# Kernel tuning notes

Measured on AMD Instinct MI355X. Metric: run time of the kernel, lower is better.

## Reference

```python
import jax, jax.numpy as jnp
import numpy as np

MEMORY_SIZE = 32768
FEATURE_DIM = 128
BATCH = 4096


def setup_inputs() -> dict:
    key = jax.random.key(0)
    k1, k2, k3, k4 = jax.random.split(key, 4)
    memory = jax.random.normal(k1, (MEMORY_SIZE, FEATURE_DIM), dtype=jnp.float32)
    input_data = jax.random.normal(k2, (BATCH, FEATURE_DIM), dtype=jnp.float32)
    write_weights = jax.random.uniform(k3, (BATCH, MEMORY_SIZE), dtype=jnp.float32)
    query = jax.random.normal(k4, (BATCH, FEATURE_DIM), dtype=jnp.float32)
    return {"memory": memory, "input_data": input_data,
            "write_weights": write_weights, "query": query}


def reference(memory, input_data, write_weights, query):
    # ---- write(): row-normalize weights, scatter-accumulate into memory ----
    # The original python double-loop computes update[j] += w[i,j] * x[i],
    # i.e. update = w_norm.T @ x  -- a single GEMM.
    w_norm = write_weights / jnp.sum(write_weights, axis=1, keepdims=True)
    update = jnp.einsum('bm,bf->mf', w_norm, input_data)  # [M, F]
    memory_new = memory + update

    # ---- read(): softmax attention over memory slots ----
    scores = jnp.matmul(query, memory_new.T)              # [B, M]
    attention_weights = jax.nn.softmax(scores, axis=1)
    retrieved_memory = jnp.matmul(attention_weights, memory_new)  # [B, F]
    confidence_scores = jnp.max(attention_weights, axis=1)        # [B]
    return retrieved_memory, confidence_scores, memory_new
```

## Files before the change

kernel.cpp:

```cpp
#include <hip/hip_runtime.h>
#include <hip/hip_bf16.h>
#include <math.h>

#define MEMSZ 32768
#define FDIM  128
#define BATCH 4096

typedef float f32x4 __attribute__((ext_vector_type(4)));
typedef _Float16 f16x8 __attribute__((ext_vector_type(8)));
typedef short bf16x8 __attribute__((ext_vector_type(8)));
typedef unsigned short u16t;
typedef unsigned int u32t;

static __device__ __forceinline__ u16t f2h_bits(float f) {
    union { _Float16 h; u16t u; } c;
    c.h = (_Float16)f;
    return c.u;
}

#define GLDS16(gsrc, ldst) \
  __builtin_amdgcn_global_load_lds((const __attribute__((address_space(1))) void*)(gsrc), \
                                   (__attribute__((address_space(3))) void*)(ldst), 16, 0, 0)

__global__ __launch_bounds__(256) void k_rowsum(const float* __restrict__ W,
                                                float* __restrict__ inv_s) {
    const int row = blockIdx.x;
    const float4* Wr = reinterpret_cast<const float4*>(W + (size_t)row * MEMSZ);
    float acc = 0.f;
    #pragma unroll 4
    for (int i = threadIdx.x; i < MEMSZ / 4; i += 256) {
        float4 v = Wr[i];
        acc += (v.x + v.y) + (v.z + v.w);
    }
    #pragma unroll
    for (int off = 32; off > 0; off >>= 1)
        acc += __shfl_down(acc, off, 64);
    __shared__ float wsum[4];
    const int lane = threadIdx.x & 63, wid = threadIdx.x >> 6;
    if (lane == 0) wsum[wid] = acc;
    __syncthreads();
    if (threadIdx.x == 0)
        inv_s[row] = 1.0f / (wsum[0] + wsum[1] + wsum[2] + wsum[3]);
}

__global__ __launch_bounds__(256) void k_prep(const float* __restrict__ X,
                                              const float* __restrict__ inv_s,
                                              unsigned char* __restrict__ XT64) {
    __shared__ float xs[64][132];
    const int T = blockIdx.x;
    const int b0 = T * 64;
    const int tid = threadIdx.x;
    #pragma unroll
    for (int i = 0; i < 8; ++i) {
        const int idx = tid + i * 256;
        const int row = idx >> 5, c4 = idx & 31;
        const float s = inv_s[b0 + row];
        float4 v = *reinterpret_cast<const float4*>(&X[(size_t)(b0 + row) * FDIM + c4 * 4]);
        v.x *= s; v.y *= s; v.z *= s; v.w *= s;
        *reinterpret_cast<float4*>(&xs[row][c4 * 4]) = v;
    }
    __syncthreads();
    #pragma unroll
    for (int i = 0; i < 4; ++i) {
        const int L = tid + i * 256;
        const int fh = L >> 9, ff = (L >> 7) & 3, ks = (L >> 6) & 1, ln = L & 63;
        const int f = fh * 64 + ff * 16 + (ln & 15);
        const int bi = ks * 32 + (ln >> 4) * 8;
        u32t pk[4];
        #pragma unroll
        for (int h = 0; h < 4; ++h) {
            const float lo = xs[bi + 2 * h][f];
            const float hi = xs[bi + 2 * h + 1][f];
            asm("v_cvt_pk_bf16_f32 %0, %1, %2" : "=v"(pk[h]) : "v"(lo), "v"(hi));
        }
        *reinterpret_cast<uint4*>(XT64 + (size_t)T * 16384 + (size_t)L * 16) =
            make_uint4(pk[0], pk[1], pk[2], pk[3]);
    }
}

#define K2B 64
#define K2M 64
__global__ __launch_bounds__(256, 2) void k_update_mfma(
    const float* __restrict__ W, const unsigned char* __restrict__ XT64,
    const float* __restrict__ Mem, float* __restrict__ MemNew,
    u16t* __restrict__ MemH, u16t* __restrict__ MemHT)
{
    __shared__ __align__(16) unsigned char wt[2][16384];

    const int tid = threadIdx.x;
    const int lane = tid & 63, w = tid >> 6;
    const int q16 = lane & 15, g = lane >> 4;
    const int wm = w >> 1, wf = w & 1;
    const int mblk = blockIdx.x * K2M;

    f32x4 acc[2][4];
    #pragma unroll
    for (int mf = 0; mf < 2; ++mf)
        #pragma unroll
        for (int ff = 0; ff < 4; ++ff) acc[mf][ff] = (f32x4){0.f, 0.f, 0.f, 0.f};

    const unsigned char* xbase = XT64 + (size_t)(wf * 8192 + lane * 16);

    auto stageW = [&](int buf, int t) {
        const int b0 = t * K2B;
        #pragma unroll
        for (int c = 0; c < 4; ++c) {
            const int gi = c * 256 + tid;
            const int b = gi >> 4;
            const int src = ((gi & 15) * 16) ^ ((b & 8) << 1);
            GLDS16((const unsigned char*)W + (size_t)(b0 + b) * (MEMSZ * 4) + (size_t)mblk * 4 + src,
                   &wt[buf][gi * 16]);
        }
    };
    auto loadB = [&](bf16x8 (&br)[4][2], int t) {
        const unsigned char* xp = xbase + (size_t)t * 16384;
        #pragma unroll
        for (int ff = 0; ff < 4; ++ff)
            #pragma unroll
            for (int ks = 0; ks < 2; ++ks)
                br[ff][ks] = *reinterpret_cast<const bf16x8*>(xp + ff * 2048 + ks * 1024);
    };
    auto compute = [&](int buf, bf16x8 (&br)[4][2]) {
        bf16x8 afr[2][2];
        const unsigned char* tb = &wt[buf][0];
        #pragma unroll
        for (int mf = 0; mf < 2; ++mf) {
            const int mm4 = (wm * 32 + mf * 16 + q16) * 4;
            #pragma unroll
            for (int ks = 0; ks < 2; ++ks) {
                float av[8];
                #pragma unroll
                for (int e = 0; e < 8; ++e) {
                    const int b = ks * 32 + g * 8 + e;
                    av[e] = *reinterpret_cast<const float*>(
                        tb + b * 256 + (mm4 ^ ((b & 8) << 1)));
                }
                union { u32t u[4]; bf16x8 v; } cv;
                #pragma unroll
                for (int h = 0; h < 4; ++h)
                    asm("v_cvt_pk_bf16_f32 %0, %1, %2" : "=v"(cv.u[h]) : "v"(av[2 * h]), "v"(av[2 * h + 1]));
                afr[mf][ks] = cv.v;
            }
        }
        #pragma unroll
        for (int mf = 0; mf < 2; ++mf)
            #pragma unroll
            for (int ff = 0; ff < 4; ++ff)
                #pragma unroll
                for (int ks = 0; ks < 2; ++ks)
                    acc[mf][ff] = __builtin_amdgcn_mfma_f32_16x16x32_bf16(
                        afr[mf][ks], br[ff][ks], acc[mf][ff], 0, 0, 0);
    };

    bf16x8 bA[4][2], bB_[4][2];
    stageW(0, 0); loadB(bA, 0);
    const int NT = BATCH / K2B;
    for (int t = 0; t < NT; t += 2) {
        __builtin_amdgcn_s_barrier();
        if (t + 1 < NT) { loadB(bB_, t + 1); stageW(1, t + 1); }
        if (t + 1 < NT) asm volatile("s_waitcnt vmcnt(12)" ::: "memory");
        else            asm volatile("s_waitcnt vmcnt(0)"  ::: "memory");
        __builtin_amdgcn_s_barrier();
        __builtin_amdgcn_sched_barrier(0);
        compute(0, bA);
        __builtin_amdgcn_s_barrier();
        if (t + 2 < NT) { loadB(bA, t + 2); stageW(0, t + 2); }
        if (t + 2 < NT) asm volatile("s_waitcnt vmcnt(12)" ::: "memory");
        else            asm volatile("s_waitcnt vmcnt(0)"  ::: "memory");
        __builtin_amdgcn_s_barrier();
        __builtin_amdgcn_sched_barrier(0);
        compute(1, bB_);
    }

    #pragma unroll
    for (int mf = 0; mf < 2; ++mf) {
        #pragma unroll
        for (int ff = 0; ff < 4; ++ff) {
            const int m0 = mblk + wm * 32 + mf * 16 + g * 4;
            const int fcol = wf * 64 + ff * 16 + q16;
            ushort4 ht;
            u16t* htp = reinterpret_cast<u16t*>(&ht);
            #pragma unroll
            for (int r = 0; r < 4; ++r) {
                const size_t idx = (size_t)(m0 + r) * FDIM + fcol;
                const float v = acc[mf][ff][r] + Mem[idx];
                MemNew[idx] = v;
                const u16t hb = f2h_bits(v);
                MemH[idx] = hb;
                htp[r] = hb;
            }
            *reinterpret_cast<ushort4*>(&MemHT[(size_t)fcol * MEMSZ + m0]) = ht;
        }
    }
}

#define K2_IT 16
#define K2_MT 64
__global__ __launch_bounds__(256) void k_update_f32(const float* __restrict__ W,
                                                    const float* __restrict__ X,
                                                    const float* __restrict__ inv_s,
                                                    const float* __restrict__ Mem,
                                                    float* __restrict__ MemNew) {
    __shared__ float w_lds[2][K2_IT][K2_MT];
    __shared__ float x_lds[2][K2_IT][FDIM];
    const int j0 = blockIdx.x * K2_MT;
    const int tid = threadIdx.x;
    const int tf = tid & 15;
    const int tj = tid >> 4;

    float acc[4][8];
    #pragma unroll
    for (int a = 0; a < 4; ++a)
        #pragma unroll
        for (int b = 0; b < 8; ++b) acc[a][b] = 0.f;

    float4 pw, px0, px1;
    float ps0, ps1;
    const int wr = tid >> 4, wc4 = tid & 15;
    const int xr0 = tid >> 5, xc0 = tid & 31;
    const int xr1 = (tid + 256) >> 5, xc1 = tid & 31;

    auto load_tile = [&](int it) {
        const int i0 = it * K2_IT;
        pw  = *reinterpret_cast<const float4*>(&W[(size_t)(i0 + wr) * MEMSZ + j0 + wc4 * 4]);
        px0 = *reinterpret_cast<const float4*>(&X[(size_t)(i0 + xr0) * FDIM + xc0 * 4]);
        ps0 = inv_s[i0 + xr0];
        px1 = *reinterpret_cast<const float4*>(&X[(size_t)(i0 + xr1) * FDIM + xc1 * 4]);
        ps1 = inv_s[i0 + xr1];
    };
    auto write_tile = [&](int buf) {
        *reinterpret_cast<float4*>(&w_lds[buf][wr][wc4 * 4]) = pw;
        float4 v = px0; v.x *= ps0; v.y *= ps0; v.z *= ps0; v.w *= ps0;
        *reinterpret_cast<float4*>(&x_lds[buf][xr0][xc0 * 4]) = v;
        float4 u = px1; u.x *= ps1; u.y *= ps1; u.z *= ps1; u.w *= ps1;
        *reinterpret_cast<float4*>(&x_lds[buf][xr1][xc1 * 4]) = u;
    };

    load_tile(0);
    write_tile(0);
    __syncthreads();
    const int NT = BATCH / K2_IT;
    for (int it = 0; it < NT; ++it) {
        const int cur = it & 1;
        if (it + 1 < NT) load_tile(it + 1);
        #pragma unroll 4
        for (int i = 0; i < K2_IT; ++i) {
            const float4 wv = *reinterpret_cast<const float4*>(&w_lds[cur][i][tj * 4]);
            const float4 xa = *reinterpret_cast<const float4*>(&x_lds[cur][i][tf * 4]);
            const float4 xb = *reinterpret_cast<const float4*>(&x_lds[cur][i][tf * 4 + 64]);
            const float wj[4] = {wv.x, wv.y, wv.z, wv.w};
            #pragma unroll
            for (int a = 0; a < 4; ++a) {
                acc[a][0] += wj[a] * xa.x; acc[a][1] += wj[a] * xa.y;
                acc[a][2] += wj[a] * xa.z; acc[a][3] += wj[a] * xa.w;
                acc[a][4] += wj[a] * xb.x; acc[a][5] += wj[a] * xb.y;
                acc[a][6] += wj[a] * xb.z; acc[a][7] += wj[a] * xb.w;
            }
        }
        if (it + 1 < NT) write_tile(cur ^ 1);
        __syncthreads();
    }
    #pragma unroll
    for (int a = 0; a < 4; ++a) {
        const size_t j = (size_t)j0 + tj * 4 + a;
        const float4 m0 = *reinterpret_cast<const float4*>(&Mem[j * FDIM + tf * 4]);
        const float4 m1 = *reinterpret_cast<const float4*>(&Mem[j * FDIM + tf * 4 + 64]);
        float4 o0 = {acc[a][0] + m0.x, acc[a][1] + m0.y, acc[a][2] + m0.z, acc[a][3] + m0.w};
        float4 o1 = {acc[a][4] + m1.x, acc[a][5] + m1.y, acc[a][6] + m1.z, acc[a][7] + m1.w};
        *reinterpret_cast<float4*>(&MemNew[j * FDIM + tf * 4]) = o0;
        *reinterpret_cast<float4*>(&MemNew[j * FDIM + tf * 4 + 64]) = o1;
    }
}

__global__ __launch_bounds__(256) void k_attn_mfma(
    const float* __restrict__ Q, const u16t* __restrict__ Kh, const u16t* __restrict__ KhT,
    float* __restrict__ accP, float* __restrict__ mP, float* __restrict__ lP, int s_shift)
{
    __shared__ __align__(16) unsigned char kv_u8[2][16384];
    __shared__ __align__(16) unsigned char v_u8[2][16384];
    __shared__ __align__(16) unsigned char p_u8[4][2048];

    const int tid = threadIdx.x;
    const int w = tid >> 6, lane = tid & 63;
    const int q16 = lane & 15, g = lane >> 4;
    const int S = 1 << s_shift;
    const int s_idx = blockIdx.x & (S - 1);
    const int qb = blockIdx.x >> s_shift;
    const int chunk = MEMSZ >> s_shift;
    const int slot0 = s_idx * chunk;
    const int NT = chunk >> 6;

    f16x8 qfrag[2][4];
    #pragma unroll
    for (int qf = 0; qf < 2; ++qf) {
        const float* qrow = Q + (size_t)(qb * 128 + w * 32 + qf * 16 + q16) * FDIM;
        #pragma unroll
        for (int ks = 0; ks < 4; ++ks) {
            float tmp[8];
            *reinterpret_cast<float4*>(&tmp[0]) = *reinterpret_cast<const float4*>(&qrow[ks * 32 + g * 8]);
            *reinterpret_cast<float4*>(&tmp[4]) = *reinterpret_cast<const float4*>(&qrow[ks * 32 + g * 8 + 4]);
            f16x8 v;
            #pragma unroll
            for (int e = 0; e < 8; ++e) v[e] = (_Float16)tmp[e];
            qfrag[qf][ks] = v;
        }
    }

    auto stage = [&](int buf, int tile) {
        const unsigned char* kbase = (const unsigned char*)Kh + (size_t)(slot0 + tile * 64) * 256;
        const unsigned char* tbase = (const unsigned char*)KhT + (size_t)(slot0 + tile * 64) * 2;
        #pragma unroll
        for (int c = 0; c < 4; ++c) {
            const int C = w * 4 + c;
            const int pp = C * 1024 + lane * 16;
            {
                const int slot = pp >> 8;
                const int inner = (pp & 255) ^ ((slot & 7) << 4);
                GLDS16(kbase + slot * 256 + inner, &kv_u8[buf][C * 1024]);
            }
            {
                const int d = pp >> 7;
                const int inner = (pp & 127) ^ ((d & 7) << 4);
                GLDS16(tbase + (size_t)d * 65536 + inner, &v_u8[buf][C * 1024]);
            }
        }
    };

    float m_run[2] = {-3.0e38f, -3.0e38f};
    float l_run[2] = {0.f, 0.f};
    f32x4 acc_o[8][2];
    #pragma unroll
    for (int df = 0; df < 8; ++df)
        #pragma unroll
        for (int qf = 0; qf < 2; ++qf)
            acc_o[df][qf] = (f32x4){0.f, 0.f, 0.f, 0.f};

    stage(0, 0);
    asm volatile("s_waitcnt vmcnt(0)" ::: "memory");
    __builtin_amdgcn_s_barrier();
    __builtin_amdgcn_sched_barrier(0);

    int cur = 0;
    for (int t = 0; t < NT; ++t) {
        if (t + 1 < NT) stage(cur ^ 1, t + 1);

        f32x4 acc_s[4][2];
        #pragma unroll
        for (int sf = 0; sf < 4; ++sf) {
            acc_s[sf][0] = (f32x4){0.f, 0.f, 0.f, 0.f};
            acc_s[sf][1] = (f32x4){0.f, 0.f, 0.f, 0.f};
        }
        const unsigned char* kvb = &kv_u8[cur][0];
        #pragma unroll
        for (int ks = 0; ks < 4; ++ks) {
            #pragma unroll
            for (int sf = 0; sf < 4; ++sf) {
                const int slot = sf * 16 + q16;
                const f16x8 a = *reinterpret_cast<const f16x8*>(
                    kvb + slot * 256 + ((ks * 64 + g * 16) ^ ((slot & 7) << 4)));
                acc_s[sf][0] = __builtin_amdgcn_mfma_f32_16x16x32_f16(a, qfrag[0][ks], acc_s[sf][0], 0, 0, 0);
                acc_s[sf][1] = __builtin_amdgcn_mfma_f32_16x16x32_f16(a, qfrag[1][ks], acc_s[sf][1], 0, 0, 0);
            }
        }

        f16x8 pb[2][2];
        unsigned char* pw = &p_u8[w][0];
        #pragma unroll
        for (int qf = 0; qf < 2; ++qf) {
            float pmax = acc_s[0][qf][0];
            #pragma unroll
            for (int sf = 0; sf < 4; ++sf)
                #pragma unroll
                for (int r = 0; r < 4; ++r)
                    pmax = fmaxf(pmax, acc_s[sf][qf][r]);
            pmax = fmaxf(pmax, __shfl_xor(pmax, 16));
            pmax = fmaxf(pmax, __shfl_xor(pmax, 32));
            const float mn = fmaxf(m_run[qf], pmax);
            float p[4][4];
            float psum = 0.f;
            #pragma unroll
            for (int sf = 0; sf < 4; ++sf)
                #pragma unroll
                for (int r = 0; r < 4; ++r) {
                    p[sf][r] = __expf(acc_s[sf][qf][r] - mn);
                    psum += p[sf][r];
                }
            psum += __shfl_xor(psum, 16);
            psum += __shfl_xor(psum, 32);
            const float sc = __expf(m_run[qf] - mn);
            l_run[qf] = l_run[qf] * sc + psum;
            m_run[qf] = mn;
            #pragma unroll
            for (int df = 0; df < 8; ++df) {
                acc_o[df][qf][0] *= sc; acc_o[df][qf][1] *= sc;
                acc_o[df][qf][2] *= sc; acc_o[df][qf][3] *= sc;
            }
            #pragma unroll
            for (int sf = 0; sf < 4; ++sf)
                #pragma unroll
                for (int rr = 0; rr < 2; ++rr) {
                    const u32t val = (u32t)f2h_bits(p[sf][2 * rr]) | ((u32t)f2h_bits(p[sf][2 * rr + 1]) << 16);
                    const int byte = q16 * 128 + (((sf * 16 + g * 4 + 2 * rr) * 2) ^ ((q16 & 7) << 4));
                    *reinterpret_cast<u32t*>(pw + byte) = val;
                }
            #pragma unroll
            for (int kk = 0; kk < 2; ++kk) {
                const int byte = q16 * 128 + (((kk * 32 + g * 8) * 2) ^ ((q16 & 7) << 4));
                pb[qf][kk] = *reinterpret_cast<const f16x8*>(pw + byte);
            }
        }

        const unsigned char* vb = &v_u8[cur][0];
        #pragma unroll
        for (int df = 0; df < 8; ++df) {
            #pragma unroll
            for (int kk = 0; kk < 2; ++kk) {
                const int d = df * 16 + q16;
                const f16x8 av = *reinterpret_cast<const f16x8*>(
                    vb + d * 128 + ((kk * 64 + g * 16) ^ ((d & 7) << 4)));
                acc_o[df][0] = __builtin_amdgcn_mfma_f32_16x16x32_f16(av, pb[0][kk], acc_o[df][0], 0, 0, 0);
                acc_o[df][1] = __builtin_amdgcn_mfma_f32_16x16x32_f16(av, pb[1][kk], acc_o[df][1], 0, 0, 0);
            }
        }

        asm volatile("s_waitcnt vmcnt(0)" ::: "memory");
        __builtin_amdgcn_s_barrier();
        __builtin_amdgcn_sched_barrier(0);
        cur ^= 1;
    }

    const int rowbase = qb * 128 + w * 32;
    #pragma unroll
    for (int qf = 0; qf < 2; ++qf) {
        const int row = rowbase + qf * 16 + q16;
        float* ap = accP + ((size_t)s_idx * BATCH + row) * FDIM;
        #pragma unroll
        for (int df = 0; df < 8; ++df) {
            float4 o = {acc_o[df][qf][0], acc_o[df][qf][1], acc_o[df][qf][2], acc_o[df][qf][3]};
            *reinterpret_cast<float4*>(&ap[df * 16 + g * 4]) = o;
        }
        if (g == 0) {
            mP[(size_t)s_idx * BATCH + row] = m_run[qf];
            lP[(size_t)s_idx * BATCH + row] = l_run[qf];
        }
    }
}

__global__ __launch_bounds__(256) void k_combine(const float* __restrict__ mP,
                                                 const float* __restrict__ lP,
                                                 const float* __restrict__ accP,
                                                 float* __restrict__ Out,
                                                 float* __restrict__ Conf, int S) {
    const int row = blockIdx.x * 8 + (threadIdx.x >> 5);
    const int lane = threadIdx.x & 31;
    float mt = -3.0e38f;
    for (int s = 0; s < S; ++s) mt = fmaxf(mt, mP[(size_t)s * BATCH + row]);
    float lt = 0.f;
    for (int s = 0; s < S; ++s) lt += lP[(size_t)s * BATCH + row] * __expf(mP[(size_t)s * BATCH + row] - mt);
    const float inv = 1.0f / lt;
    float4 o = {0.f, 0.f, 0.f, 0.f};
    for (int s = 0; s < S; ++s) {
        const float wgt = __expf(mP[(size_t)s * BATCH + row] - mt);
        const float4 a = *reinterpret_cast<const float4*>(&accP[((size_t)s * BATCH + row) * FDIM + lane * 4]);
        o.x += wgt * a.x; o.y += wgt * a.y; o.z += wgt * a.z; o.w += wgt * a.w;
    }
    float4 res = {o.x * inv, o.y * inv, o.z * inv, o.w * inv};
    *reinterpret_cast<float4*>(&Out[(size_t)row * FDIM + lane * 4]) = res;
    if (lane == 0) Conf[row] = inv;
}

#define QT 16
#define MT 64
#define LSTR (FDIM + 4)
__global__ __launch_bounds__(256) void k_attn_f32(const float* __restrict__ Q,
                                                  const float* __restrict__ MemNew,
                                                  float* __restrict__ Out,
                                                  float* __restrict__ Conf) {
    __shared__ float mem_lds[MT][LSTR];
    __shared__ float q_lds[QT][LSTR];
    __shared__ float p_lds[QT][MT];
    __shared__ float m_lds[QT], l_lds[QT], scale_lds[QT];

    const int tid = threadIdx.x;
    const int qblk = blockIdx.x * QT;

    #pragma unroll
    for (int r = 0; r < 2; ++r) {
        const int idx = tid + r * 256;
        const int row = idx >> 5, c4 = idx & 31;
        *reinterpret_cast<float4*>(&q_lds[row][c4 * 4]) =
            *reinterpret_cast<const float4*>(&Q[(size_t)(qblk + row) * FDIM + c4 * 4]);
    }
    if (tid < QT) { m_lds[tid] = -3.0e38f; l_lds[tid] = 0.f; }

    const int sq = (tid >> 5) * 2;
    const int sm = tid & 31;
    const int pq = tid >> 4;
    const int pf = (tid & 15) * 4;

    float acc[8];
    #pragma unroll
    for (int e = 0; e < 8; ++e) acc[e] = 0.f;

    for (int mt = 0; mt < MEMSZ / MT; ++mt) {
        __syncthreads();
        const float* src = MemNew + (size_t)mt * MT * FDIM;
        #pragma unroll
        for (int r = 0; r < 8; ++r) {
            const int idx = tid + r * 256;
            const int row = idx >> 5, c4 = idx & 31;
            *reinterpret_cast<float4*>(&mem_lds[row][c4 * 4]) =
                *reinterpret_cast<const float4*>(&src[(size_t)row * FDIM + c4 * 4]);
        }
        const float mold0 = m_lds[sq], mold1 = m_lds[sq + 1];
        __syncthreads();

        float s00 = 0.f, s01 = 0.f, s10 = 0.f, s11 = 0.f;
        #pragma unroll 8
        for (int k = 0; k < FDIM; k += 4) {
            const float4 qa = *reinterpret_cast<const float4*>(&q_lds[sq][k]);
            const float4 qb = *reinterpret_cast<const float4*>(&q_lds[sq + 1][k]);
            const float4 ma = *reinterpret_cast<const float4*>(&mem_lds[sm][k]);
            const float4 mb = *reinterpret_cast<const float4*>(&mem_lds[sm + 32][k]);
            s00 += qa.x*ma.x + qa.y*ma.y + qa.z*ma.z + qa.w*ma.w;
            s01 += qa.x*mb.x + qa.y*mb.y + qa.z*mb.z + qa.w*mb.w;
            s10 += qb.x*ma.x + qb.y*ma.y + qb.z*ma.z + qb.w*ma.w;
            s11 += qb.x*mb.x + qb.y*mb.y + qb.z*mb.z + qb.w*mb.w;
        }
        float r0 = fmaxf(s00, s01), r1 = fmaxf(s10, s11);
        #pragma unroll
        for (int off = 1; off <= 16; off <<= 1) {
            r0 = fmaxf(r0, __shfl_xor(r0, off, 64));
            r1 = fmaxf(r1, __shfl_xor(r1, off, 64));
        }
        const float mn0 = fmaxf(mold0, r0), mn1 = fmaxf(mold1, r1);
        const float p00 = __expf(s00 - mn0), p01 = __expf(s01 - mn0);
        const float p10 = __expf(s10 - mn1), p11 = __expf(s11 - mn1);
        float t0 = p00 + p01, t1 = p10 + p11;
        #pragma unroll
        for (int off = 1; off <= 16; off <<= 1) {
            t0 += __shfl_xor(t0, off, 64);
            t1 += __shfl_xor(t1, off, 64);
        }
        p_lds[sq][sm]      = p00; p_lds[sq][sm + 32]     = p01;
        p_lds[sq + 1][sm]  = p10; p_lds[sq + 1][sm + 32] = p11;
        if (sm == 0) {
            const float sc0 = __expf(mold0 - mn0), sc1 = __expf(mold1 - mn1);
            m_lds[sq] = mn0; m_lds[sq + 1] = mn1;
            l_lds[sq]     = l_lds[sq]     * sc0 + t0;
            l_lds[sq + 1] = l_lds[sq + 1] * sc1 + t1;
            scale_lds[sq] = sc0; scale_lds[sq + 1] = sc1;
        }
        __syncthreads();

        const float sc = scale_lds[pq];
        #pragma unroll
        for (int e = 0; e < 8; ++e) acc[e] *= sc;
        #pragma unroll 8
        for (int m = 0; m < MT; ++m) {
            const float p = p_lds[pq][m];
            const float4 va = *reinterpret_cast<const float4*>(&mem_lds[m][pf]);
            const float4 vb = *reinterpret_cast<const float4*>(&mem_lds[m][pf + 64]);
            acc[0] += p * va.x; acc[1] += p * va.y; acc[2] += p * va.z; acc[3] += p * va.w;
            acc[4] += p * vb.x; acc[5] += p * vb.y; acc[6] += p * vb.z; acc[7] += p * vb.w;
        }
    }
    const float linv = 1.0f / l_lds[pq];
    float4 o0 = {acc[0]*linv, acc[1]*linv, acc[2]*linv, acc[3]*linv};
    float4 o1 = {acc[4]*linv, acc[5]*linv, acc[6]*linv, acc[7]*linv};
    *reinterpret_cast<float4*>(&Out[(size_t)(qblk + pq) * FDIM + pf]) = o0;
    *reinterpret_cast<float4*>(&Out[(size_t)(qblk + pq) * FDIM + pf + 64]) = o1;
    if (tid < QT) Conf[qblk + tid] = 1.0f / l_lds[tid];
}

extern "C" void kernel_launch(void* const* d_in, const int* in_sizes, int n_in,
                              void* d_out, int out_size, void* d_ws, size_t ws_size,
                              hipStream_t stream) {
    (void)in_sizes; (void)n_in; (void)out_size;
    const float* memory   = (const float*)d_in[0];
    const float* input    = (const float*)d_in[1];
    const float* wweights = (const float*)d_in[2];
    const float* query    = (const float*)d_in[3];

    float* out       = (float*)d_out;
    float* retrieved = out;
    float* conf      = out + (size_t)BATCH * FDIM;
    float* mem_new   = conf + BATCH;

    char* ws = (char*)d_ws;
    float* inv_s = (float*)ws;
    const size_t off_xt   = 16384;
    const size_t off_h    = off_xt + (size_t)FDIM * BATCH * 2;
    const size_t off_hT   = off_h + (size_t)MEMSZ * FDIM * 2;
    const size_t off_part = off_hT + (size_t)MEMSZ * FDIM * 2;

    int s_shift = -1;
    for (int sh = 4; sh >= 0; --sh) {
        const size_t S = (size_t)1 << sh;
        const size_t need = off_part + S * ((size_t)BATCH * 8 + (size_t)BATCH * FDIM * 4);
        if (ws_size >= need) { s_shift = sh; break; }
    }

    k_rowsum<<<BATCH, 256, 0, stream>>>(wweights, inv_s);
    if (s_shift >= 0) {
        const int S = 1 << s_shift;
        unsigned char* xt64 = (unsigned char*)(ws + off_xt);
        u16t* mh  = (u16t*)(ws + off_h);
        u16t* mhT = (u16t*)(ws + off_hT);
        float* mP   = (float*)(ws + off_part);
        float* lP   = mP + (size_t)S * BATCH;
        float* accP = lP + (size_t)S * BATCH;
        k_prep<<<BATCH / 64, 256, 0, stream>>>(input, inv_s, xt64);
        k_update_mfma<<<MEMSZ / K2M, 256, 0, stream>>>(wweights, xt64, memory, mem_new, mh, mhT);
        k_attn_mfma<<<(BATCH / 128) * S, 256, 0, stream>>>(query, mh, mhT, accP, mP, lP, s_shift);
        k_combine<<<BATCH / 8, 256, 0, stream>>>(mP, lP, accP, retrieved, conf, S);
    } else {
        k_update_f32<<<MEMSZ / K2_MT, 256, 0, stream>>>(wweights, input, inv_s, memory, mem_new);
        k_attn_f32<<<BATCH / QT, 256, 0, stream>>>(query, mem_new, retrieved, conf);
    }
}
```

Measured before the change: 399.3 us.

## Split-K the memory update GEMM into two halves with a finalize kernel

Adds a split-K variant of the write-update GEMM that runs twice as many blocks, each covering half of the batch dimension and writing fp32 partials to a workspace. A separate finalize kernel sums memory plus both partials and emits the fp32 new memory along with its fp16 and transposed fp16 copies. The goal is more parallelism and occupancy on the update GEMM. In exchange it adds an extra launch and extra global traffic for the partials, and it is used only when the workspace is large enough.

```diff
diff --git a/kernel.cpp b/kernel.cpp
--- a/kernel.cpp
+++ b/kernel.cpp
@@ -80,6 +80,149 @@
 
 #define K2B 64
 #define K2M 64
+__global__ __launch_bounds__(256, 4) void k_update_sk(
+    const float* __restrict__ W, const unsigned char* __restrict__ XT64,
+    float* __restrict__ P)
+{
+    __shared__ __align__(16) unsigned char wt[2][16384];
+
+    const int tid = threadIdx.x;
+    const int lane = tid & 63, w = tid >> 6;
+    const int q16 = lane & 15, g = lane >> 4;
+    const int wm = w >> 1, wf = w & 1;
+    const int mblk = (blockIdx.x >> 1) * K2M;
+    const int khalf = blockIdx.x & 1;
+    const int base = khalf * 32;
+
+    f32x4 acc[2][4];
+    #pragma unroll
+    for (int mf = 0; mf < 2; ++mf)
+        #pragma unroll
+        for (int ff = 0; ff < 4; ++ff) acc[mf][ff] = (f32x4){0.f, 0.f, 0.f, 0.f};
+
+    const unsigned char* xbase = XT64 + (size_t)(wf * 8192 + lane * 16);
+
+    auto stageW = [&](int buf, int t) {
+        const int b0 = t * K2B;
+        #pragma unroll
+        for (int c = 0; c < 4; ++c) {
+            const int gi = c * 256 + tid;
+            const int b = gi >> 4;
+            const int src = ((gi & 15) * 16) ^ ((b & 8) << 1);
+            GLDS16((const unsigned char*)W + (size_t)(b0 + b) * (MEMSZ * 4) + (size_t)mblk * 4 + src,
+                   &wt[buf][gi * 16]);
+        }
+    };
+    auto loadB = [&](bf16x8 (&br)[4][2], int t) {
+        const unsigned char* xp = xbase + (size_t)t * 16384;
+        #pragma unroll
+        for (int ff = 0; ff < 4; ++ff)
+            #pragma unroll
+            for (int ks = 0; ks < 2; ++ks)
+                br[ff][ks] = *reinterpret_cast<const bf16x8*>(xp + ff * 2048 + ks * 1024);
+    };
+    auto compute = [&](int buf, bf16x8 (&br)[4][2]) {
+        bf16x8 afr[2][2];
+        const unsigned char* tb = &wt[buf][0];
+        #pragma unroll
+        for (int mf = 0; mf < 2; ++mf) {
+            const int mm4 = (wm * 32 + mf * 16 + q16) * 4;
+            #pragma unroll
+            for (int ks = 0; ks < 2; ++ks) {
+                float av[8];
+                #pragma unroll
+                for (int e = 0; e < 8; ++e) {
+                    const int b = ks * 32 + g * 8 + e;
+                    av[e] = *reinterpret_cast<const float*>(
+                        tb + b * 256 + (mm4 ^ ((b & 8) << 1)));
+                }
+                union { u32t u[4]; bf16x8 v; } cv;
+                #pragma unroll
+                for (int h = 0; h < 4; ++h)
+                    asm("v_cvt_pk_bf16_f32 %0, %1, %2" : "=v"(cv.u[h]) : "v"(av[2 * h]), "v"(av[2 * h + 1]));
+                afr[mf][ks] = cv.v;
+            }
+        }
+        #pragma unroll
+        for (int mf = 0; mf < 2; ++mf)
+            #pragma unroll
+            for (int ff = 0; ff < 4; ++ff)
+                #pragma unroll
+                for (int ks = 0; ks < 2; ++ks)
+                    acc[mf][ff] = __builtin_amdgcn_mfma_f32_16x16x32_bf16(
+                        afr[mf][ks], br[ff][ks], acc[mf][ff], 0, 0, 0);
+    };
+
+    bf16x8 bA[4][2], bB_[4][2];
+    stageW(0, base); loadB(bA, base);
+    const int NT = 32;
+    for (int t = 0; t < NT; t += 2) {
+        __builtin_amdgcn_s_barrier();
+        if (t + 1 < NT) {
+            loadB(bB_, base + t + 1); stageW(1, base + t + 1);
+            asm volatile("s_waitcnt vmcnt(12)" ::: "memory");
+        } else asm volatile("s_waitcnt vmcnt(0)" ::: "memory");
+        __builtin_amdgcn_s_barrier();
+        __builtin_amdgcn_sched_barrier(0);
+        compute(0, bA);
+        __builtin_amdgcn_s_barrier();
+        if (t + 2 < NT) {
+            loadB(bA, base + t + 2); stageW(0, base + t + 2);
+            asm volatile("s_waitcnt vmcnt(12)" ::: "memory");
+        } else asm volatile("s_waitcnt vmcnt(0)" ::: "memory");
+        __builtin_amdgcn_s_barrier();
+        __builtin_amdgcn_sched_barrier(0);
+        compute(1, bB_);
+    }
+
+    float* Pk = P + (size_t)khalf * MEMSZ * FDIM;
+    #pragma unroll
+    for (int mf = 0; mf < 2; ++mf) {
+        #pragma unroll
+        for (int ff = 0; ff < 4; ++ff) {
+            const int m0 = mblk + wm * 32 + mf * 16 + g * 4;
+            const int fcol = wf * 64 + ff * 16 + q16;
+            #pragma unroll
+            for (int r = 0; r < 4; ++r)
+                Pk[(size_t)(m0 + r) * FDIM + fcol] = acc[mf][ff][r];
+        }
+    }
+}
+
+__global__ __launch_bounds__(256) void k_fin(const float* __restrict__ Mem,
+                                             const float* __restrict__ P,
+                                             float* __restrict__ MemNew,
+                                             u16t* __restrict__ MemH,
+                                             u16t* __restrict__ MemHT) {
+    const int tid = threadIdx.x;
+    const int lane = tid & 63, w = tid >> 6;
+    const int q16 = lane & 15, g = lane >> 4;
+    const int wm = w >> 1, wf = w & 1;
+    const int mblk = blockIdx.x * 64;
+    const float* P0 = P;
+    const float* P1 = P + (size_t)MEMSZ * FDIM;
+    #pragma unroll
+    for (int mf = 0; mf < 2; ++mf) {
+        #pragma unroll
+        for (int ff = 0; ff < 4; ++ff) {
+            const int m0 = mblk + wm * 32 + mf * 16 + g * 4;
+            const int fcol = wf * 64 + ff * 16 + q16;
+            ushort4 ht;
+            u16t* htp = reinterpret_cast<u16t*>(&ht);
+            #pragma unroll
+            for (int r = 0; r < 4; ++r) {
+                const size_t idx = (size_t)(m0 + r) * FDIM + fcol;
+                const float v = Mem[idx] + P0[idx] + P1[idx];
+                MemNew[idx] = v;
+                const u16t hb = f2h_bits(v);
+                MemH[idx] = hb;
+                htp[r] = hb;
+            }
+            *reinterpret_cast<ushort4*>(&MemHT[(size_t)fcol * MEMSZ + m0]) = ht;
+        }
+    }
+}
+
 __global__ __launch_bounds__(256, 2) void k_update_mfma(
     const float* __restrict__ W, const unsigned char* __restrict__ XT64,
     const float* __restrict__ Mem, float* __restrict__ MemNew,
@@ -593,6 +736,27 @@
     const size_t off_h    = off_xt + (size_t)FDIM * BATCH * 2;
     const size_t off_hT   = off_h + (size_t)MEMSZ * FDIM * 2;
     const size_t off_part = off_hT + (size_t)MEMSZ * FDIM * 2;
+    const size_t sz_p16   = (size_t)16 * ((size_t)BATCH * 8 + (size_t)BATCH * FDIM * 4);
+    const size_t off_pk   = off_part + sz_p16;
+    const size_t need_full = off_pk + (size_t)2 * MEMSZ * FDIM * 4;
+
+    k_rowsum<<<BATCH, 256, 0, stream>>>(wweights, inv_s);
+
+    if (ws_size >= need_full) {
+        unsigned char* xt64 = (unsigned char*)(ws + off_xt);
+        u16t* mh  = (u16t*)(ws + off_h);
+        u16t* mhT = (u16t*)(ws + off_hT);
+        float* mP   = (float*)(ws + off_part);
+        float* lP   = mP + (size_t)16 * BATCH;
+        float* accP = lP + (size_t)16 * BATCH;
+        float* pk   = (float*)(ws + off_pk);
+        k_prep<<<BATCH / 64, 256, 0, stream>>>(input, inv_s, xt64);
+        k_update_sk<<<(MEMSZ / K2M) * 2, 256, 0, stream>>>(wweights, xt64, pk);
+        k_fin<<<MEMSZ / 64, 256, 0, stream>>>(memory, pk, mem_new, mh, mhT);
+        k_attn_mfma<<<(BATCH / 128) * 16, 256, 0, stream>>>(query, mh, mhT, accP, mP, lP, 4);
+        k_combine<<<BATCH / 8, 256, 0, stream>>>(mP, lP, accP, retrieved, conf, 16);
+        return;
+    }
 
     int s_shift = -1;
     for (int sh = 4; sh >= 0; --sh) {
@@ -600,8 +764,6 @@
         const size_t need = off_part + S * ((size_t)BATCH * 8 + (size_t)BATCH * FDIM * 4);
         if (ws_size >= need) { s_shift = sh; break; }
     }
-
-    k_rowsum<<<BATCH, 256, 0, stream>>>(wweights, inv_s);
     if (s_shift >= 0) {
         const int S = 1 << s_shift;
         unsigned char* xt64 = (unsigned char*)(ws + off_xt);
```

New measurement: 455.0 us. 13.9% more time.
